# Optimization experiments

Measured on AMD Instinct MI355X. Metric: run time of the kernel, lower is better.

The kernel has to match this reference:

```python
import jax, jax.numpy as jnp
import numpy as np

B, H, S, D = 4, 8, 2048, 64
NEG = -1e9


def setup_inputs() -> dict:
    key = jax.random.key(0)
    k1, k2, k3, k4 = jax.random.split(key, 4)
    qs = jax.random.normal(k1, (B, H, S, D), dtype=jnp.float32)
    ks = jax.random.normal(k2, (B, H, S, D), dtype=jnp.float32)
    vs = jax.random.normal(k3, (B, H, S, D), dtype=jnp.float32)
    # binary 0/1 float mask, broadcast over heads
    mask = (jax.random.uniform(k4, (B, 1, S, S)) < 0.5).astype(jnp.float32)
    return {"qs": qs, "ks": ks, "vs": vs, "mask": mask}


def reference(qs, ks, vs, mask):
    scale = 1.0 / np.sqrt(qs.shape[-1]).astype(np.float32)
    # [B,H,S,S] logits; multiplicative pre-mask, then additive -1e9 on masked slots
    logits = jnp.einsum('bhqd,bhkd->bhqk', qs, ks) * mask * scale
    logits = logits + (1.0 - mask) * NEG
    weights = jax.nn.softmax(logits, axis=-1) * mask  # multiplicative post-mask
    return jnp.einsum('bhqk,bhkd->bhqd', weights, vs)
```

## Files before the change

### kernel.cpp

```cpp
#include <hip/hip_runtime.h>
#include <stdint.h>

#define S_LEN 2048
#define NTILE 32

typedef float f32x4 __attribute__((ext_vector_type(4)));
typedef float f32x16 __attribute__((ext_vector_type(16)));
typedef short bf16x8 __attribute__((ext_vector_type(8)));

__device__ __forceinline__ uint16_t f2bf(float f) {
    uint32_t u = __float_as_uint(f);
    return (uint16_t)((u + 0x7FFFu + ((u >> 16) & 1u)) >> 16);
}

#define AS3PTR(p) ((__attribute__((address_space(3))) uint32_t*)(uintptr_t)(p))
#define AS1PTR(p) ((const __attribute__((address_space(1))) uint32_t*)(uintptr_t)(p))

__global__ __launch_bounds__(256)
void prep_all(const float* __restrict__ K, const float* __restrict__ V,
              const float* __restrict__ M, uint8_t* __restrict__ Kd,
              uint8_t* __restrict__ Vd, uint16_t* __restrict__ Mp)
{
    __shared__ float mt[4096];
    const int bid = blockIdx.x;
    const int tid = threadIdx.x;
    if (bid < 2048) {
        int flat = bid * 256 + tid;
        int s = flat & 511, tile = flat >> 9;
        int key = s >> 3, dc = (s >> 1) & 3, h = s & 1;
        int kt = tile & 31, bh = tile >> 5;
        const float* src = K + (((size_t)bh * S_LEN + kt * 64 + key) << 6) + dc * 16 + h * 8;
        f32x4 a = *(const f32x4*)src;
        f32x4 b = *(const f32x4*)(src + 4);
        bf16x8 o;
        o[0] = (short)f2bf(a[0]); o[1] = (short)f2bf(a[1]);
        o[2] = (short)f2bf(a[2]); o[3] = (short)f2bf(a[3]);
        o[4] = (short)f2bf(b[0]); o[5] = (short)f2bf(b[1]);
        o[6] = (short)f2bf(b[2]); o[7] = (short)f2bf(b[3]);
        *(bf16x8*)(Kd + ((size_t)tile << 13) + (((dc * 2 + h) * 64 + key) << 4)) = o;
    } else if (bid < 4096) {
        int flat = (bid - 2048) * 256 + tid;
        int s = flat & 511, tile = flat >> 9;
        int d = s & 63, h = (s >> 6) & 1, ku = s >> 7;
        int kt = tile & 31, bh = tile >> 5;
        const float* src = V + (((size_t)bh * S_LEN + kt * 64 + ku * 16 + h * 8) << 6) + d;
        bf16x8 o;
        #pragma unroll
        for (int j = 0; j < 8; ++j) o[j] = (short)f2bf(src[j << 6]);
        *(bf16x8*)(Vd + ((size_t)tile << 13) + (((ku * 2 + h) * 64 + d) << 4)) = o;
    } else {
        int mid = bid - 4096;
        int b = mid >> 10, qt = (mid >> 5) & 31, kt = mid & 31;
        int row = tid >> 2, cc = tid & 3;
        const float* src = M + ((size_t)(b * S_LEN + qt * 64 + row) * S_LEN) + kt * 64;
        #pragma unroll
        for (int i = 0; i < 4; ++i)
            *(f32x4*)&mt[(row << 6) + cc * 16 + i * 4] =
                *(const f32x4*)(src + cc * 16 + i * 4);
        __syncthreads();
        int l = tid & 63, w = tid >> 6;
        int qw = w >> 1, kw = w & 1, h = l >> 5, l31 = l & 31;
        uint32_t m = 0;
        #pragma unroll
        for (int r = 0; r < 16; ++r) {
            int keyl = 32 * kw + (r & 3) + 8 * (r >> 2) + 4 * h;
            m |= (mt[((32 * qw + l31) << 6) + keyl] > 0.5f) << r;
        }
        Mp[((size_t)mid << 8) + tid] = (uint16_t)m;
    }
}

#define K_OFF 0
#define V_OFF 16384

__global__ __launch_bounds__(256, 4)
void attn_fwd(const float* __restrict__ Q, const uint8_t* __restrict__ Kd,
              const uint8_t* __restrict__ Vd, const uint16_t* __restrict__ Mp,
              float* __restrict__ O)
{
    __shared__ __align__(16) uint8_t lds[32768];

    const int tid  = threadIdx.x;
    const int lane = tid & 63;
    const int w    = tid >> 6;
    const int qw   = w >> 1;
    const int kw   = w & 1;
    const int h    = lane >> 5;
    const int l31  = lane & 31;

    const int bid0 = blockIdx.x;
    const int bid  = ((bid0 & 7) << 7) + (bid0 >> 3);
    const int bh  = bid >> 5;
    const int qt  = bid & 31;
    const int b   = bh >> 3;
    const int q0  = qt << 6;

    const float QSCL = 0.125f * 1.44269504088896340736f;
    bf16x8 qf[4];
    {
        const float* qrow = Q + (((size_t)bh * S_LEN + q0 + 32 * qw + l31) << 6);
        #pragma unroll
        for (int dc = 0; dc < 4; ++dc) {
            f32x4 a  = *(const f32x4*)(qrow + dc * 16 + h * 8);
            f32x4 b4 = *(const f32x4*)(qrow + dc * 16 + h * 8 + 4);
            bf16x8 f;
            f[0] = (short)f2bf(a[0] * QSCL);  f[1] = (short)f2bf(a[1] * QSCL);
            f[2] = (short)f2bf(a[2] * QSCL);  f[3] = (short)f2bf(a[3] * QSCL);
            f[4] = (short)f2bf(b4[0] * QSCL); f[5] = (short)f2bf(b4[1] * QSCL);
            f[6] = (short)f2bf(b4[2] * QSCL); f[7] = (short)f2bf(b4[3] * QSCL);
            qf[dc] = f;
        }
    }

    f32x16 acc[2];
    acc[0] = (f32x16)(0.f);
    acc[1] = (f32x16)(0.f);
    float lsum = 0.f;

    const uint8_t*  ktb = Kd + (((size_t)bh * 32) << 13);
    const uint8_t*  vtb = Vd + (((size_t)bh * 32) << 13);
    const uint16_t* mbase = Mp + (((size_t)(b * 32 + qt) * 32) << 8) + (w << 6) + lane;

    auto stage = [&](int buf, int t) {
        #pragma unroll
        for (int i = 0; i < 2; ++i) {
            int off = (i << 12) + (w << 10);
            __builtin_amdgcn_global_load_lds(
                AS1PTR(ktb + ((size_t)t << 13) + off + lane * 16),
                AS3PTR(&lds[K_OFF + (buf << 13) + off]), 16, 0, 0);
            __builtin_amdgcn_global_load_lds(
                AS1PTR(vtb + ((size_t)t << 13) + off + lane * 16),
                AS3PTR(&lds[V_OFF + (buf << 13) + off]), 16, 0, 0);
        }
    };

    stage(0, 0);
    __syncthreads();

    #pragma unroll 2
    for (int kt = 0; kt < NTILE; ++kt) {
        const int buf = kt & 1;
        if (kt + 1 < NTILE) stage(buf ^ 1, kt + 1);

        uint32_t mw = mbase[kt << 8];

        const uint8_t* kb = &lds[K_OFF + (buf << 13)];
        f32x16 s = (f32x16)(0.f);
        #pragma unroll
        for (int dc = 0; dc < 4; ++dc) {
            bf16x8 kf = *(const bf16x8*)(kb + (((dc * 2 + h) * 64 + 32 * kw + l31) << 4));
            s = __builtin_amdgcn_mfma_f32_32x32x16_bf16(kf, qf[dc], s, 0, 0, 0);
        }

        uint32_t pd[8];
        #pragma unroll
        for (int rq = 0; rq < 8; ++rq) {
            float x0 = (mw & (1u << (2 * rq)))     ? s[2 * rq]     : -1000.f;
            float x1 = (mw & (1u << (2 * rq + 1))) ? s[2 * rq + 1] : -1000.f;
            float e0, e1;
            asm("v_exp_f32 %0, %1" : "=v"(e0) : "v"(x0));
            asm("v_exp_f32 %0, %1" : "=v"(e1) : "v"(x1));
            lsum += e0 + e1;
            asm("v_cvt_pk_bf16_f32 %0, %1, %2" : "=v"(pd[rq]) : "v"(e0), "v"(e1));
        }

        #pragma unroll
        for (int u = 0; u < 2; ++u) {
            asm("v_permlane32_swap_b32 %0, %1" : "+v"(pd[4 * u]),     "+v"(pd[4 * u + 2]));
            asm("v_permlane32_swap_b32 %0, %1" : "+v"(pd[4 * u + 1]), "+v"(pd[4 * u + 3]));
        }

        const uint8_t* vbuf = &lds[V_OFF + (buf << 13)];
        #pragma unroll
        for (int u = 0; u < 2; ++u) {
            union { uint32_t d[4]; bf16x8 v; } pa;
            pa.d[0] = pd[4 * u]; pa.d[1] = pd[4 * u + 1];
            pa.d[2] = pd[4 * u + 2]; pa.d[3] = pd[4 * u + 3];
            #pragma unroll
            for (int dblk = 0; dblk < 2; ++dblk) {
                bf16x8 vf = *(const bf16x8*)(vbuf +
                    ((((kw * 2 + u) * 2 + h) * 64 + 32 * dblk + l31) << 4));
                acc[dblk] = __builtin_amdgcn_mfma_f32_32x32x16_bf16(pa.v, vf, acc[dblk], 0, 0, 0);
            }
        }

        __syncthreads();
    }

    lsum += __shfl_xor(lsum, 32, 64);

    float* ex  = (float*)lds;
    float* ex2 = (float*)(lds + 16384);
    if (kw == 1) {
        #pragma unroll
        for (int dblk = 0; dblk < 2; ++dblk)
            #pragma unroll
            for (int rq = 0; rq < 4; ++rq) {
                f32x4 v = { acc[dblk][4 * rq], acc[dblk][4 * rq + 1],
                            acc[dblk][4 * rq + 2], acc[dblk][4 * rq + 3] };
                *(f32x4*)&ex[(qw << 11) + (((dblk << 2) + rq) << 8) + (lane << 2)] = v;
            }
        if (lane < 32) ex2[(qw << 5) + lane] = lsum;
    }
    __syncthreads();
    if (kw == 0) {
        #pragma unroll
        for (int dblk = 0; dblk < 2; ++dblk)
            #pragma unroll
            for (int rq = 0; rq < 4; ++rq) {
                f32x4 v = *(const f32x4*)&ex[(qw << 11) + (((dblk << 2) + rq) << 8) + (lane << 2)];
                acc[dblk][4 * rq]     += v[0];
                acc[dblk][4 * rq + 1] += v[1];
                acc[dblk][4 * rq + 2] += v[2];
                acc[dblk][4 * rq + 3] += v[3];
            }
        float l = lsum + ex2[(qw << 5) + l31];
        float linv = (l > 0.f) ? 1.f / l : 0.f;

        float* obase = O + (((size_t)bh * S_LEN + q0 + 32 * qw) << 6);
        #pragma unroll
        for (int r = 0; r < 16; ++r) {
            int qloc = (r & 3) + 8 * (r >> 2) + 4 * h;
            float inv = __shfl(linv, qloc, 64);
            obase[(qloc << 6) + l31]      = acc[0][r] * inv;
            obase[(qloc << 6) + 32 + l31] = acc[1][r] * inv;
        }
    }
}

extern "C" void kernel_launch(void* const* d_in, const int* in_sizes, int n_in,
                              void* d_out, int out_size, void* d_ws, size_t ws_size,
                              hipStream_t stream) {
    const float* qs   = (const float*)d_in[0];
    const float* ks   = (const float*)d_in[1];
    const float* vs   = (const float*)d_in[2];
    const float* mask = (const float*)d_in[3];
    float* out = (float*)d_out;
    (void)in_sizes; (void)n_in; (void)out_size; (void)ws_size;

    uint8_t* ws = (uint8_t*)d_ws;
    uint8_t* Kd = ws;
    uint8_t* Vd = ws + (8u << 20);
    uint16_t* Mp = (uint16_t*)(ws + (16u << 20));

    hipLaunchKernelGGL(prep_all, dim3(8192), dim3(256), 0, stream,
                       ks, vs, mask, Kd, Vd, Mp);
    hipLaunchKernelGGL(attn_fwd, dim3(1024), dim3(256), 0, stream,
                       qs, Kd, Vd, Mp, out);
}
```

Baseline: 79.29 us.

## Split key range across two blocks with partial-sum reduction kernel

Adds a KSPLIT template so each attention block processes half the key tiles, doubling the grid to 2048 blocks. Unnormalized partial numerators and row sums go to workspace, and a new reduce_o kernel combines them and normalizes. It also raises the launch-bounds occupancy hint to 5 and wraps the MFMA sections with s_setprio. The aim is better CU occupancy and load balance, paid for with an extra launch and roughly 32MB of partial-output traffic. This is safe without max-rescaling only because the softmax uses fixed-offset exponentials.

```diff
diff --git a/kernel.cpp b/kernel.cpp
--- a/kernel.cpp
+++ b/kernel.cpp
@@ -73,9 +73,11 @@
 #define K_OFF 0
 #define V_OFF 16384
 
-__global__ __launch_bounds__(256, 4)
+template <int KSPLIT>
+__global__ __launch_bounds__(256, 5)
 void attn_fwd(const float* __restrict__ Q, const uint8_t* __restrict__ Kd,
               const uint8_t* __restrict__ Vd, const uint16_t* __restrict__ Mp,
+              float* __restrict__ numP, float* __restrict__ lsumP,
               float* __restrict__ O)
 {
     __shared__ __align__(16) uint8_t lds[32768];
@@ -88,12 +90,17 @@
     const int h    = lane >> 5;
     const int l31  = lane & 31;
 
+    const int NB   = 1024 * KSPLIT;
     const int bid0 = blockIdx.x;
-    const int bid  = ((bid0 & 7) << 7) + (bid0 >> 3);
-    const int bh  = bid >> 5;
-    const int qt  = bid & 31;
+    const int bid  = (bid0 & 7) * (NB >> 3) + (bid0 >> 3);
+    const int bh    = bid / (32 * KSPLIT);
+    const int rest  = bid % (32 * KSPLIT);
+    const int qt    = rest / KSPLIT;
+    const int khalf = rest % KSPLIT;
     const int b   = bh >> 3;
     const int q0  = qt << 6;
+    const int NT    = NTILE / KSPLIT;
+    const int kt0   = khalf * NT;
 
     const float QSCL = 0.125f * 1.44269504088896340736f;
     bf16x8 qf[4];
@@ -134,23 +141,26 @@
         }
     };
 
-    stage(0, 0);
+    stage(0, kt0);
     __syncthreads();
 
     #pragma unroll 2
-    for (int kt = 0; kt < NTILE; ++kt) {
-        const int buf = kt & 1;
-        if (kt + 1 < NTILE) stage(buf ^ 1, kt + 1);
+    for (int tt = 0; tt < NT; ++tt) {
+        const int kt  = kt0 + tt;
+        const int buf = tt & 1;
+        if (tt + 1 < NT) stage(buf ^ 1, kt + 1);
 
         uint32_t mw = mbase[kt << 8];
 
         const uint8_t* kb = &lds[K_OFF + (buf << 13)];
         f32x16 s = (f32x16)(0.f);
+        __builtin_amdgcn_s_setprio(1);
         #pragma unroll
         for (int dc = 0; dc < 4; ++dc) {
             bf16x8 kf = *(const bf16x8*)(kb + (((dc * 2 + h) * 64 + 32 * kw + l31) << 4));
             s = __builtin_amdgcn_mfma_f32_32x32x16_bf16(kf, qf[dc], s, 0, 0, 0);
         }
+        __builtin_amdgcn_s_setprio(0);
 
         uint32_t pd[8];
         #pragma unroll
@@ -171,6 +181,7 @@
         }
 
         const uint8_t* vbuf = &lds[V_OFF + (buf << 13)];
+        __builtin_amdgcn_s_setprio(1);
         #pragma unroll
         for (int u = 0; u < 2; ++u) {
             union { uint32_t d[4]; bf16x8 v; } pa;
@@ -183,6 +194,7 @@
                 acc[dblk] = __builtin_amdgcn_mfma_f32_32x32x16_bf16(pa.v, vf, acc[dblk], 0, 0, 0);
             }
         }
+        __builtin_amdgcn_s_setprio(0);
 
         __syncthreads();
     }
@@ -215,17 +227,47 @@
                 acc[dblk][4 * rq + 3] += v[3];
             }
         float l = lsum + ex2[(qw << 5) + l31];
-        float linv = (l > 0.f) ? 1.f / l : 0.f;
-
-        float* obase = O + (((size_t)bh * S_LEN + q0 + 32 * qw) << 6);
-        #pragma unroll
-        for (int r = 0; r < 16; ++r) {
-            int qloc = (r & 3) + 8 * (r >> 2) + 4 * h;
-            float inv = __shfl(linv, qloc, 64);
-            obase[(qloc << 6) + l31]      = acc[0][r] * inv;
-            obase[(qloc << 6) + 32 + l31] = acc[1][r] * inv;
-        }
-    }
+
+        if (KSPLIT == 1) {
+            float linv = (l > 0.f) ? 1.f / l : 0.f;
+            float* obase = O + (((size_t)bh * S_LEN + q0 + 32 * qw) << 6);
+            #pragma unroll
+            for (int r = 0; r < 16; ++r) {
+                int qloc = (r & 3) + 8 * (r >> 2) + 4 * h;
+                float inv = __shfl(linv, qloc, 64);
+                obase[(qloc << 6) + l31]      = acc[0][r] * inv;
+                obase[(qloc << 6) + 32 + l31] = acc[1][r] * inv;
+            }
+        } else {
+            size_t pb = (size_t)(bh * 32 + qt) * KSPLIT + khalf;
+            if (h == 0) lsumP[(pb << 6) + (qw << 5) + l31] = l;
+            float* nb = numP + (pb << 12) + (qw << 11);
+            #pragma unroll
+            for (int r = 0; r < 16; ++r) {
+                int qloc = (r & 3) + 8 * (r >> 2) + 4 * h;
+                nb[(qloc << 6) + l31]      = acc[0][r];
+                nb[(qloc << 6) + 32 + l31] = acc[1][r];
+            }
+        }
+    }
+}
+
+__global__ __launch_bounds__(256)
+void reduce_o(const float* __restrict__ numP, const float* __restrict__ lsumP,
+              float* __restrict__ O)
+{
+    int i  = blockIdx.x * 256 + threadIdx.x;
+    int d4 = i & 15;
+    int q  = (i >> 4) & 2047;
+    int bh = i >> 15;
+    int qt = q >> 6, ql = q & 63;
+    size_t pb = (size_t)(bh * 32 + qt) * 2;
+    f32x4 a = *(const f32x4*)(numP + (pb << 12) + (ql << 6) + (d4 << 2));
+    f32x4 c = *(const f32x4*)(numP + ((pb + 1) << 12) + (ql << 6) + (d4 << 2));
+    float l = lsumP[(pb << 6) + ql] + lsumP[((pb + 1) << 6) + ql];
+    float inv = (l > 0.f) ? 1.f / l : 0.f;
+    f32x4 o = (a + c) * inv;
+    *(f32x4*)(O + ((size_t)i << 2)) = o;
 }
 
 extern "C" void kernel_launch(void* const* d_in, const int* in_sizes, int n_in,
@@ -236,15 +278,26 @@
     const float* vs   = (const float*)d_in[2];
     const float* mask = (const float*)d_in[3];
     float* out = (float*)d_out;
-    (void)in_sizes; (void)n_in; (void)out_size; (void)ws_size;
+    (void)in_sizes; (void)n_in; (void)out_size;
 
     uint8_t* ws = (uint8_t*)d_ws;
     uint8_t* Kd = ws;
     uint8_t* Vd = ws + (8u << 20);
     uint16_t* Mp = (uint16_t*)(ws + (16u << 20));
+    float* numP  = (float*)(ws + (18u << 20));
+    float* lsumP = (float*)(ws + (18u << 20) + 2048ull * 4096 * 4);
+
+    const size_t need = (18u << 20) + 2048ull * 4096 * 4 + 2048ull * 64 * 4;
 
     hipLaunchKernelGGL(prep_all, dim3(8192), dim3(256), 0, stream,
                        ks, vs, mask, Kd, Vd, Mp);
-    hipLaunchKernelGGL(attn_fwd, dim3(1024), dim3(256), 0, stream,
-                       qs, Kd, Vd, Mp, out);
-}
+    if (ws_size >= need) {
+        hipLaunchKernelGGL((attn_fwd<2>), dim3(2048), dim3(256), 0, stream,
+                           qs, Kd, Vd, Mp, numP, lsumP, out);
+        hipLaunchKernelGGL(reduce_o, dim3(4096), dim3(256), 0, stream,
+                           numP, lsumP, out);
+    } else {
+        hipLaunchKernelGGL((attn_fwd<1>), dim3(1024), dim3(256), 0, stream,
+                           qs, Kd, Vd, Mp, (float*)nullptr, (float*)nullptr, out);
+    }
+}
```

New measurement: 108.9 us. 1.37x slower.

## Triple-buffer K/V tiles with explicit vmcnt waits and MFMA priority hints

Applied to the files above, without the earlier changes.

Replaces the double-buffered K/V staging with a three-slot LDS ring, prefetching two tiles ahead and prefetching the mask word into registers alongside each stage. The single end-of-iteration barrier becomes a partial vmcnt wait plus barrier at the top of each step, and s_setprio raises wave priority around the MFMA sections. The aim is to hide global-load latency more deeply and overlap softmax work with other waves' matrix ops. In exchange, LDS use grows to 48KB and the occupancy hint drops from 4 to 3 blocks per CU.

```diff
diff --git a/kernel.cpp b/kernel.cpp
--- a/kernel.cpp
+++ b/kernel.cpp
@@ -70,15 +70,12 @@
     }
 }
 
-#define K_OFF 0
-#define V_OFF 16384
-
-__global__ __launch_bounds__(256, 4)
+__global__ __launch_bounds__(256, 3)
 void attn_fwd(const float* __restrict__ Q, const uint8_t* __restrict__ Kd,
               const uint8_t* __restrict__ Vd, const uint16_t* __restrict__ Mp,
               float* __restrict__ O)
 {
-    __shared__ __align__(16) uint8_t lds[32768];
+    __shared__ __align__(16) uint8_t lds[49152];
 
     const int tid  = threadIdx.x;
     const int lane = tid & 63;
@@ -117,78 +114,100 @@
     acc[1] = (f32x16)(0.f);
     float lsum = 0.f;
 
-    const uint8_t*  ktb = Kd + (((size_t)bh * 32) << 13);
-    const uint8_t*  vtb = Vd + (((size_t)bh * 32) << 13);
+    const uint8_t*  ksrc  = Kd + (((size_t)bh * 32) << 13) + (w << 10) + lane * 16;
+    const uint8_t*  vsrc  = Vd + (((size_t)bh * 32) << 13) + (w << 10) + lane * 16;
     const uint16_t* mbase = Mp + (((size_t)(b * 32 + qt) * 32) << 8) + (w << 6) + lane;
 
-    auto stage = [&](int buf, int t) {
-        #pragma unroll
-        for (int i = 0; i < 2; ++i) {
-            int off = (i << 12) + (w << 10);
-            __builtin_amdgcn_global_load_lds(
-                AS1PTR(ktb + ((size_t)t << 13) + off + lane * 16),
-                AS3PTR(&lds[K_OFF + (buf << 13) + off]), 16, 0, 0);
-            __builtin_amdgcn_global_load_lds(
-                AS1PTR(vtb + ((size_t)t << 13) + off + lane * 16),
-                AS3PTR(&lds[V_OFF + (buf << 13) + off]), 16, 0, 0);
-        }
-    };
-
-    stage(0, 0);
+    uint32_t mreg[3];
+
+#define STAGE(T, SLOT)                                                          \
+    {                                                                           \
+        size_t toff = (size_t)(T) << 13;                                        \
+        __builtin_amdgcn_global_load_lds(AS1PTR(ksrc + toff),                   \
+            AS3PTR(&lds[(SLOT) * 16384 + (w << 10)]), 16, 0, 0);                \
+        __builtin_amdgcn_global_load_lds(AS1PTR(ksrc + toff + 4096),            \
+            AS3PTR(&lds[(SLOT) * 16384 + 4096 + (w << 10)]), 16, 0, 0);         \
+        __builtin_amdgcn_global_load_lds(AS1PTR(vsrc + toff),                   \
+            AS3PTR(&lds[(SLOT) * 16384 + 8192 + (w << 10)]), 16, 0, 0);         \
+        __builtin_amdgcn_global_load_lds(AS1PTR(vsrc + toff + 4096),            \
+            AS3PTR(&lds[(SLOT) * 16384 + 12288 + (w << 10)]), 16, 0, 0);        \
+        mreg[SLOT] = mbase[(size_t)(T) << 8];                                   \
+    }
+
+#define COMPUTE(B)                                                              \
+    {                                                                           \
+        const uint8_t* kb   = &lds[(B) * 16384];                                \
+        const uint8_t* vbuf = &lds[(B) * 16384 + 8192];                         \
+        uint32_t mw = mreg[B];                                                  \
+        f32x16 s = (f32x16)(0.f);                                               \
+        __builtin_amdgcn_s_setprio(1);                                          \
+        _Pragma("unroll")                                                       \
+        for (int dc = 0; dc < 4; ++dc) {                                        \
+            bf16x8 kf = *(const bf16x8*)(kb + (((dc * 2 + h) * 64 + 32 * kw + l31) << 4)); \
+            s = __builtin_amdgcn_mfma_f32_32x32x16_bf16(kf, qf[dc], s, 0, 0, 0); \
+        }                                                                       \
+        __builtin_amdgcn_s_setprio(0);                                          \
+        uint32_t pd[8];                                                         \
+        _Pragma("unroll")                                                       \
+        for (int rq = 0; rq < 8; ++rq) {                                        \
+            float x0 = (mw & (1u << (2 * rq)))     ? s[2 * rq]     : -1000.f;   \
+            float x1 = (mw & (1u << (2 * rq + 1))) ? s[2 * rq + 1] : -1000.f;   \
+            float e0, e1;                                                       \
+            asm("v_exp_f32 %0, %1" : "=v"(e0) : "v"(x0));                       \
+            asm("v_exp_f32 %0, %1" : "=v"(e1) : "v"(x1));                       \
+            lsum += e0 + e1;                                                    \
+            asm("v_cvt_pk_bf16_f32 %0, %1, %2" : "=v"(pd[rq]) : "v"(e0), "v"(e1)); \
+        }                                                                       \
+        _Pragma("unroll")                                                       \
+        for (int u = 0; u < 2; ++u) {                                           \
+            asm("v_permlane32_swap_b32 %0, %1" : "+v"(pd[4*u]),   "+v"(pd[4*u+2])); \
+            asm("v_permlane32_swap_b32 %0, %1" : "+v"(pd[4*u+1]), "+v"(pd[4*u+3])); \
+        }                                                                       \
+        __builtin_amdgcn_s_setprio(1);                                          \
+        _Pragma("unroll")                                                       \
+        for (int u = 0; u < 2; ++u) {                                           \
+            union { uint32_t d[4]; bf16x8 v; } pa;                              \
+            pa.d[0] = pd[4*u]; pa.d[1] = pd[4*u+1];                             \
+            pa.d[2] = pd[4*u+2]; pa.d[3] = pd[4*u+3];                           \
+            _Pragma("unroll")                                                   \
+            for (int dblk = 0; dblk < 2; ++dblk) {                              \
+                bf16x8 vf = *(const bf16x8*)(vbuf +                             \
+                    ((((kw * 2 + u) * 2 + h) * 64 + 32 * dblk + l31) << 4));    \
+                acc[dblk] = __builtin_amdgcn_mfma_f32_32x32x16_bf16(pa.v, vf, acc[dblk], 0, 0, 0); \
+            }                                                                   \
+        }                                                                       \
+        __builtin_amdgcn_s_setprio(0);                                          \
+    }
+
+#define BODY(T, B, SLOT2, WN, DOSTAGE)                                          \
+    {                                                                           \
+        asm volatile("s_waitcnt vmcnt(" #WN ")" ::: "memory");                  \
+        __builtin_amdgcn_s_barrier();                                           \
+        __builtin_amdgcn_sched_barrier(0);                                      \
+        if (DOSTAGE) STAGE((T) + 2, SLOT2);                                     \
+        COMPUTE(B);                                                             \
+    }
+
+    STAGE(0, 0);
+    STAGE(1, 1);
+
+    #pragma unroll 1
+    for (int it = 0; it < 10; ++it) {
+        int t = it * 3;
+        BODY(t,     0, 2, 5, true);
+        BODY(t + 1, 1, 0, 5, true);
+        BODY(t + 2, 2, 1, 5, true);
+    }
+    BODY(30, 0, 2, 5, false);
+    BODY(31, 1, 2, 0, false);
+
+#undef BODY
+#undef COMPUTE
+#undef STAGE
+
+    lsum += __shfl_xor(lsum, 32, 64);
+
     __syncthreads();
-
-    #pragma unroll 2
-    for (int kt = 0; kt < NTILE; ++kt) {
-        const int buf = kt & 1;
-        if (kt + 1 < NTILE) stage(buf ^ 1, kt + 1);
-
-        uint32_t mw = mbase[kt << 8];
-
-        const uint8_t* kb = &lds[K_OFF + (buf << 13)];
-        f32x16 s = (f32x16)(0.f);
-        #pragma unroll
-        for (int dc = 0; dc < 4; ++dc) {
-            bf16x8 kf = *(const bf16x8*)(kb + (((dc * 2 + h) * 64 + 32 * kw + l31) << 4));
-            s = __builtin_amdgcn_mfma_f32_32x32x16_bf16(kf, qf[dc], s, 0, 0, 0);
-        }
-
-        uint32_t pd[8];
-        #pragma unroll
-        for (int rq = 0; rq < 8; ++rq) {
-            float x0 = (mw & (1u << (2 * rq)))     ? s[2 * rq]     : -1000.f;
-            float x1 = (mw & (1u << (2 * rq + 1))) ? s[2 * rq + 1] : -1000.f;
-            float e0, e1;
-            asm("v_exp_f32 %0, %1" : "=v"(e0) : "v"(x0));
-            asm("v_exp_f32 %0, %1" : "=v"(e1) : "v"(x1));
-            lsum += e0 + e1;
-            asm("v_cvt_pk_bf16_f32 %0, %1, %2" : "=v"(pd[rq]) : "v"(e0), "v"(e1));
-        }
-
-        #pragma unroll
-        for (int u = 0; u < 2; ++u) {
-            asm("v_permlane32_swap_b32 %0, %1" : "+v"(pd[4 * u]),     "+v"(pd[4 * u + 2]));
-            asm("v_permlane32_swap_b32 %0, %1" : "+v"(pd[4 * u + 1]), "+v"(pd[4 * u + 3]));
-        }
-
-        const uint8_t* vbuf = &lds[V_OFF + (buf << 13)];
-        #pragma unroll
-        for (int u = 0; u < 2; ++u) {
-            union { uint32_t d[4]; bf16x8 v; } pa;
-            pa.d[0] = pd[4 * u]; pa.d[1] = pd[4 * u + 1];
-            pa.d[2] = pd[4 * u + 2]; pa.d[3] = pd[4 * u + 3];
-            #pragma unroll
-            for (int dblk = 0; dblk < 2; ++dblk) {
-                bf16x8 vf = *(const bf16x8*)(vbuf +
-                    ((((kw * 2 + u) * 2 + h) * 64 + 32 * dblk + l31) << 4));
-                acc[dblk] = __builtin_amdgcn_mfma_f32_32x32x16_bf16(pa.v, vf, acc[dblk], 0, 0, 0);
-            }
-        }
-
-        __syncthreads();
-    }
-
-    lsum += __shfl_xor(lsum, 32, 64);
-
     float* ex  = (float*)lds;
     float* ex2 = (float*)(lds + 16384);
     if (kw == 1) {
```

New measurement: 80.36 us. About the same (+1.3%).
